# Kernel tuning notes

Hardware: AMD Instinct MI355X
Metric: run time of the kernel (lower is better)

Reference implementation:

```python
import jax, jax.numpy as jnp
import numpy as np


def setup_inputs() -> dict:
    key = jax.random.key(0)
    k1, k2 = jax.random.split(key)
    B, N, D = 16, 2048, 256
    candidate_vector = jax.random.normal(k1, (B, N, D), dtype=jnp.float32)
    # lengths in [1, N] so every softmax row has at least one valid column
    length = jax.random.randint(k2, (B,), 1, N + 1, dtype=jnp.int64)
    return {"candidate_vector": candidate_vector, "length": length}


def reference(candidate_vector, length):
    # scores[b,i,j] = <x_bi, x_bj>   (B, N, N)
    scores = jnp.einsum('bid,bjd->bij', candidate_vector, candidate_vector)
    # torch mask: mask[b,i,j] = (j < length[b]) -> columns past length masked
    N = candidate_vector.shape[1]
    col_valid = jnp.arange(N)[None, None, :] < length[:, None, None]  # (B,1,N)->(B,N,N) broadcast
    scores = jnp.where(col_valid, scores, -jnp.inf)
    weights = jax.nn.softmax(scores, axis=2)
    return jnp.einsum('bij,bjd->bid', weights, candidate_vector)
```

## Files before the change

### kernel.cpp

```cpp
#include <hip/hip_runtime.h>
#include <hip/hip_fp16.h>
#include <math.h>

typedef _Float16 f16;
typedef __attribute__((ext_vector_type(8))) _Float16 f16x8;
typedef __attribute__((ext_vector_type(4))) _Float16 f16x4;
typedef __attribute__((ext_vector_type(4))) float f32x4;
typedef unsigned int u32;
typedef unsigned long long u64;

#define NB 16
#define NN 2048
#define ND 256
#define KVB 32
#define QB 64
#define XSZ ((size_t)NB * NN * ND)

__device__ __forceinline__ void gll16(const void* g, void* l) {
    __builtin_amdgcn_global_load_lds(
        (const __attribute__((address_space(1))) unsigned int*)g,
        (__attribute__((address_space(3))) unsigned int*)l, 16, 0, 0);
}

__device__ __forceinline__ long long len_at(const int* lenp, int b, bool is64) {
    return is64 ? ((const long long*)lenp)[b] : (long long)lenp[b];
}

__device__ __forceinline__ float bperm_f(int src_lane, float v) {
    return __int_as_float(__builtin_amdgcn_ds_bpermute(src_lane * 4, __float_as_int(v)));
}

__global__ __launch_bounds__(256)
void prep(const float* __restrict__ X, f16* __restrict__ Xh, f16* __restrict__ Xt)
{
    const int b  = blockIdx.z;
    const int n0 = blockIdx.x * 64;
    const int d0 = blockIdx.y * 64;
    const int t  = threadIdx.x;
    __shared__ f16 T[64][72];

    const float* Xb  = X  + ((size_t)b*NN + n0)*ND + d0;
    f16*         Xhb = Xh + ((size_t)b*NN + n0)*ND + d0;
    #pragma unroll
    for (int it = 0; it < 4; ++it) {
        int r  = it*16 + (t >> 4);
        int c4 = t & 15;
        float4 v = *(const float4*)(Xb + (size_t)r*ND + c4*4);
        f16x4 h; h[0]=(f16)v.x; h[1]=(f16)v.y; h[2]=(f16)v.z; h[3]=(f16)v.w;
        *(f16x4*)&Xhb[(size_t)r*ND + c4*4] = h;
        *(f16x4*)&T[r][c4*4] = h;
    }
    __syncthreads();
    f16* Xtb = Xt + ((size_t)b*ND + d0)*NN + n0;
    #pragma unroll
    for (int it = 0; it < 2; ++it) {
        int id = it*256 + t;
        int dr = id >> 3;
        int ch = id & 7;
        f16x8 v;
        #pragma unroll
        for (int u = 0; u < 8; ++u) v[u] = T[ch*8+u][dr];
        *(f16x8*)&Xtb[(size_t)dr*NN + ch*8] = v;
    }
}

__global__ __launch_bounds__(256, 2)
void attn12(const f16* __restrict__ Xh, const f16* __restrict__ Xt,
            const int* __restrict__ lenp,
            f16* __restrict__ Op, float* __restrict__ Sl)
{
    const int tid  = threadIdx.x;
    const int lane = tid & 63;
    const int w = tid >> 6;
    const int g = lane >> 4;
    const int c = lane & 15;

    const bool is64 = (lenp[1] == 0);
    long long Lv[NB];
    #pragma unroll
    for (int i = 0; i < NB; ++i) Lv[i] = len_at(lenp, i, is64);
    const int x   = blockIdx.x & 7;
    const int kk2 = blockIdx.x >> 3;
    const int h   = kk2 & 1;
    const int k2  = kk2 >> 1;
    const int wanted = (k2 < 32) ? x : (15 - x);
    const int qt  = k2 & 31;
    int bsel = 0; long long Lb = 1;
    #pragma unroll
    for (int bb = 0; bb < NB; ++bb) {
        int rk = 0;
        #pragma unroll
        for (int b2 = 0; b2 < NB; ++b2)
            rk += (Lv[b2] > Lv[bb]) || (Lv[b2] == Lv[bb] && b2 < bb);
        if (rk == wanted) { bsel = bb; Lb = Lv[bb]; }
    }
    const int nt  = (int)((Lb + KVB - 1) / KVB);
    const int nth = (h == 0) ? ((nt + 1) >> 1) : (nt >> 1);
    if (nth == 0) return;

    __shared__ f16 Kl[8192];
    __shared__ f16 Vl[8192];
    __shared__ f16 Pl[4][16*40];

    const char* xhb = (const char*)(Xh + (size_t)bsel*NN*ND);
    const char* xtb = (const char*)(Xt + (size_t)bsel*ND*NN);

    f16x8 qf[8];
    {
        const char* qp = xhb + (size_t)(qt*QB + w*16 + c)*512 + g*16;
        const f16 LOG2E = (f16)1.44269504f;
        #pragma unroll
        for (int kk = 0; kk < 8; ++kk) {
            f16x8 v = *(const f16x8*)(qp + kk*64);
            qf[kk] = v * LOG2E;
        }
    }

    u64   ksrc[4], vsrc[4];
    char* kdst[4];
    char* vdst[4];
    {
        #pragma unroll
        for (int it = 0; it < 4; ++it) {
            int S  = it*256 + tid;
            int kk = S >> 7, j = (S >> 2) & 31, gg = S & 3;
            ksrc[it] = (u64)(xhb + (size_t)(h*KVB + j)*512 + kk*64 + gg*16);
            kdst[it] = (char*)&Kl[0] + S*16;
            int dt = S >> 6, cc = (S >> 2) & 15, g2 = S & 3;
            vsrc[it] = (u64)(xtb + (size_t)(dt*16 + cc)*4096 + (size_t)(h*KVB + g2*8)*2);
            vdst[it] = (char*)&Vl[0] + S*16;
        }
    }
    auto stage_k = [&]() {
        #pragma unroll
        for (int it = 0; it < 4; ++it) {
            gll16((const void*)ksrc[it], kdst[it]);
            ksrc[it] += (u64)(2*KVB*512);
        }
    };
    auto stage_v = [&]() {
        #pragma unroll
        for (int it = 0; it < 4; ++it) {
            gll16((const void*)vsrc[it], vdst[it]);
            vsrc[it] += (u64)(2*KVB*2);
        }
    };

    f32x4 o[16];
    #pragma unroll
    for (int dt = 0; dt < 16; ++dt) o[dt] = (f32x4){0.f,0.f,0.f,0.f};
    float m = -INFINITY;
    float l = 0.f;

    f16* pw = &Pl[w][0];

    stage_k();
    stage_v();

    for (int ti = 0; ti < nth; ++ti) {
        const int kv0 = (2*ti + h) * KVB;
        const bool more = (ti + 1 < nth);

        asm volatile("s_waitcnt vmcnt(4)" ::: "memory");
        __builtin_amdgcn_s_barrier();

        const char* kb = (const char*)&Kl[0];
        const char* vb = (const char*)&Vl[0];

        f32x4 s0 = (f32x4){0.f,0.f,0.f,0.f};
        f32x4 s1 = (f32x4){0.f,0.f,0.f,0.f};
        __builtin_amdgcn_s_setprio(1);
        #pragma unroll
        for (int kk = 0; kk < 8; ++kk) {
            f16x8 b0 = *(const f16x8*)(kb + kk*2048        + c*64 + g*16);
            f16x8 b1 = *(const f16x8*)(kb + kk*2048 + 1024 + c*64 + g*16);
            s0 = __builtin_amdgcn_mfma_f32_16x16x32_f16(b0, qf[kk], s0, 0, 0, 0);
            s1 = __builtin_amdgcn_mfma_f32_16x16x32_f16(b1, qf[kk], s1, 0, 0, 0);
        }
        __builtin_amdgcn_s_setprio(0);

        asm volatile("s_waitcnt vmcnt(0)" ::: "memory");
        __builtin_amdgcn_s_barrier();
        if (more) stage_k();

        const float NEG = -1e30f;
        if (kv0 + KVB > (int)Lb) {
            const int jb = kv0 + g*4;
            #pragma unroll
            for (int r = 0; r < 4; ++r) {
                if (jb + r >= Lb)      s0[r] = NEG;
                if (jb + 16 + r >= Lb) s1[r] = NEG;
            }
        }

        float tm = fmaxf(fmaxf(fmaxf(s0[0],s0[1]), fmaxf(s0[2],s0[3])),
                         fmaxf(fmaxf(s1[0],s1[1]), fmaxf(s1[2],s1[3])));
        tm = fmaxf(tm, __shfl_xor(tm, 16, 64));
        tm = fmaxf(tm, __shfl_xor(tm, 32, 64));
        if (__any(tm > m + 11.54f)) {
            float mn = fmaxf(m, tm);
            float sc = exp2f(m - mn);
            m = mn; l *= sc;
            float scr[4];
            #pragma unroll
            for (int r = 0; r < 4; ++r) scr[r] = bperm_f(g*4 + r, sc);
            #pragma unroll
            for (int dt = 0; dt < 16; ++dt) {
                o[dt][0]*=scr[0]; o[dt][1]*=scr[1]; o[dt][2]*=scr[2]; o[dt][3]*=scr[3];
            }
        }
        float p0[4], p1[4];
        #pragma unroll
        for (int r = 0; r < 4; ++r) {
            p0[r] = exp2f(s0[r] - m);
            p1[r] = exp2f(s1[r] - m);
        }
        float rs = ((p0[0]+p0[1]) + (p0[2]+p0[3])) + ((p1[0]+p1[1]) + (p1[2]+p1[3]));
        rs += __shfl_xor(rs, 16, 64);
        rs += __shfl_xor(rs, 32, 64);
        l += rs;

        f16x4 pa, pb;
        pa[0]=(f16)p0[0]; pa[1]=(f16)p0[1]; pa[2]=(f16)p0[2]; pa[3]=(f16)p0[3];
        pb[0]=(f16)p1[0]; pb[1]=(f16)p1[1]; pb[2]=(f16)p1[2]; pb[3]=(f16)p1[3];
        *(f16x4*)&pw[c*40 + 4*g]      = pa;
        *(f16x4*)&pw[c*40 + 16 + 4*g] = pb;
        f16x8 pf = *(const f16x8*)&pw[c*40 + 8*g];

        __builtin_amdgcn_s_setprio(1);
        #pragma unroll
        for (int dt = 0; dt < 16; ++dt) {
            f16x8 vf = *(const f16x8*)(vb + dt*1024 + c*64 + g*16);
            o[dt] = __builtin_amdgcn_mfma_f32_16x16x32_f16(pf, vf, o[dt], 0, 0, 0);
        }
        __builtin_amdgcn_s_setprio(0);

        asm volatile("" ::: "memory");
        __builtin_amdgcn_s_barrier();
        if (more) stage_v();
    }

    float linv = 1.f / l;
    float inv[4];
    #pragma unroll
    for (int r = 0; r < 4; ++r) inv[r] = bperm_f(g*4 + r, linv);
    f16* op = Op + (size_t)h*XSZ + ((size_t)bsel*NN + (size_t)(qt*QB + w*16 + g*4))*ND + c;
    #pragma unroll
    for (int r = 0; r < 4; ++r) {
        #pragma unroll
        for (int dt = 0; dt < 16; ++dt)
            op[(size_t)r*ND + dt*16] = (f16)(o[dt][r] * inv[r]);
    }
    if (g == 0) {
        Sl[((size_t)(h*NB + bsel))*NN + (size_t)(qt*QB + w*16 + c)] = m + log2f(l);
    }
}

__global__ __launch_bounds__(256)
void merge(const f16* __restrict__ Op, const float* __restrict__ Sl,
           const int* __restrict__ lenp, float* __restrict__ out)
{
    const int tid = threadIdx.x;
    const int rg  = blockIdx.x * 8 + (tid >> 5);
    const int b   = rg >> 11;
    const int q   = rg & 2047;
    const int d0  = (tid & 31) * 8;

    const bool is64 = (lenp[1] == 0);
    const long long Lb = len_at(lenp, b, is64);

    const f16* p1 = Op + ((size_t)b*NN + q)*ND + d0;
    f16x8 a1 = *(const f16x8*)p1;
    float r[8];
    if (Lb <= KVB) {
        #pragma unroll
        for (int i = 0; i < 8; ++i) r[i] = (float)a1[i];
    } else {
        f16x8 a2 = *(const f16x8*)(p1 + XSZ);
        float s1 = Sl[(size_t)b*NN + q];
        float s2 = Sl[(size_t)(NB + b)*NN + q];
        float sm = fmaxf(s1, s2);
        float w1 = exp2f(s1 - sm), w2 = exp2f(s2 - sm);
        float dn = 1.f / (w1 + w2);
        w1 *= dn; w2 *= dn;
        #pragma unroll
        for (int i = 0; i < 8; ++i) r[i] = (float)a1[i]*w1 + (float)a2[i]*w2;
    }
    float* ob = out + ((size_t)b*NN + q)*ND + d0;
    *(float4*)ob       = (float4){r[0], r[1], r[2], r[3]};
    *(float4*)(ob + 4) = (float4){r[4], r[5], r[6], r[7]};
}

__global__ __launch_bounds__(256, 2)
void attn4(const f16* __restrict__ Xh, const f16* __restrict__ Xt,
           const int* __restrict__ lenp, float* __restrict__ out)
{
    const int tid  = threadIdx.x;
    const int lane = tid & 63;
    const int w = tid >> 6;
    const int g = lane >> 4;
    const int c = lane & 15;

    const bool is64 = (lenp[1] == 0);
    long long Lv[NB];
    #pragma unroll
    for (int i = 0; i < NB; ++i) Lv[i] = len_at(lenp, i, is64);
    const int x = blockIdx.x & 7;
    const int k = blockIdx.x >> 3;
    const int wanted = (k < 32) ? x : (15 - x);
    const int qt = k & 31;
    int bsel = 0; long long Lb = 1;
    #pragma unroll
    for (int bb = 0; bb < NB; ++bb) {
        int rk = 0;
        #pragma unroll
        for (int b2 = 0; b2 < NB; ++b2)
            rk += (Lv[b2] > Lv[bb]) || (Lv[b2] == Lv[bb] && b2 < bb);
        if (rk == wanted) { bsel = bb; Lb = Lv[bb]; }
    }
    const int nt = (int)((Lb + KVB - 1) / KVB);

    __shared__ f16 Kl[2][8192];
    __shared__ f16 Vl[2][8192];
    __shared__ f16 Pl[4][16*36];

    const char* xhb = (const char*)(Xh + (size_t)bsel*NN*ND);
    const char* xtb = (const char*)(Xt + (size_t)bsel*ND*NN);

    f16x8 qf[8];
    {
        const char* qp = xhb + (size_t)(qt*QB + w*16 + c)*512 + g*16;
        #pragma unroll
        for (int kk = 0; kk < 8; ++kk) qf[kk] = *(const f16x8*)(qp + kk*64);
    }

    auto stage = [&](int buf, int kv0) {
        char* kb = (char*)&Kl[buf][0];
        char* vb = (char*)&Vl[buf][0];
        #pragma unroll
        for (int it = 0; it < 4; ++it) {
            int S  = it*256 + tid;
            int kk = S >> 7, j = (S >> 2) & 31, gg = S & 3;
            gll16(xhb + (size_t)(kv0 + j)*512 + kk*64 + gg*16, kb + S*16);
        }
        #pragma unroll
        for (int it = 0; it < 4; ++it) {
            int T  = it*256 + tid;
            int dt = T >> 6, cc = (T >> 2) & 15, gg = T & 3;
            gll16(xtb + (size_t)(dt*16 + cc)*4096 + (size_t)(kv0 + gg*8)*2, vb + T*16);
        }
    };

    f32x4 o[16];
    #pragma unroll
    for (int dt = 0; dt < 16; ++dt) o[dt] = (f32x4){0.f,0.f,0.f,0.f};
    float m[4] = {-INFINITY,-INFINITY,-INFINITY,-INFINITY};
    float l[4] = {0.f,0.f,0.f,0.f};

    f16* pw = &Pl[w][0];

    stage(0, 0);
    if (nt > 1) stage(1, KVB);

    for (int t = 0; t < nt; ++t) {
        const int kv0 = t * KVB;
        const int buf = t & 1;

        if (t + 1 < nt) { asm volatile("s_waitcnt vmcnt(8)" ::: "memory"); }
        else            { asm volatile("s_waitcnt vmcnt(0)" ::: "memory"); }
        __builtin_amdgcn_s_barrier();

        const char* kb = (const char*)&Kl[buf][0];
        const char* vb = (const char*)&Vl[buf][0];

        f32x4 s0 = (f32x4){0.f,0.f,0.f,0.f};
        f32x4 s1 = (f32x4){0.f,0.f,0.f,0.f};
        #pragma unroll
        for (int kk = 0; kk < 8; ++kk) {
            f16x8 b0 = *(const f16x8*)(kb + kk*2048        + c*64 + g*16);
            f16x8 b1 = *(const f16x8*)(kb + kk*2048 + 1024 + c*64 + g*16);
            s0 = __builtin_amdgcn_mfma_f32_16x16x32_f16(qf[kk], b0, s0, 0, 0, 0);
            s1 = __builtin_amdgcn_mfma_f32_16x16x32_f16(qf[kk], b1, s1, 0, 0, 0);
        }

        const float NEG = -1e30f;
        if (kv0 + c >= Lb)      { s0[0]=NEG; s0[1]=NEG; s0[2]=NEG; s0[3]=NEG; }
        if (kv0 + 16 + c >= Lb) { s1[0]=NEG; s1[1]=NEG; s1[2]=NEG; s1[3]=NEG; }

        float mx[4], mn[4], sc[4], p0[4], p1[4], rs[4];
        #pragma unroll
        for (int r = 0; r < 4; ++r) mx[r] = fmaxf(s0[r], s1[r]);
        #pragma unroll
        for (int off = 8; off >= 1; off >>= 1) {
            #pragma unroll
            for (int r = 0; r < 4; ++r)
                mx[r] = fmaxf(mx[r], __shfl_xor(mx[r], off, 64));
        }
        #pragma unroll
        for (int r = 0; r < 4; ++r) {
            mn[r] = fmaxf(m[r], mx[r]);
            sc[r] = __expf(m[r] - mn[r]);
            p0[r] = __expf(s0[r] - mn[r]);
            p1[r] = __expf(s1[r] - mn[r]);
            rs[r] = p0[r] + p1[r];
        }
        #pragma unroll
        for (int off = 8; off >= 1; off >>= 1) {
            #pragma unroll
            for (int r = 0; r < 4; ++r)
                rs[r] += __shfl_xor(rs[r], off, 64);
        }
        bool chg = (sc[0]!=1.f) | (sc[1]!=1.f) | (sc[2]!=1.f) | (sc[3]!=1.f);
        if (__any(chg)) {
            #pragma unroll
            for (int dt = 0; dt < 16; ++dt) {
                o[dt][0]*=sc[0]; o[dt][1]*=sc[1]; o[dt][2]*=sc[2]; o[dt][3]*=sc[3];
            }
        }
        #pragma unroll
        for (int r = 0; r < 4; ++r) { l[r] = l[r]*sc[r] + rs[r]; m[r] = mn[r]; }

        #pragma unroll
        for (int r = 0; r < 4; ++r) {
            pw[(g*4+r)*36 + c]      = (f16)p0[r];
            pw[(g*4+r)*36 + 16 + c] = (f16)p1[r];
        }
        union { f16x4 hh[2]; f16x8 v; } pu;
        pu.hh[0] = *(const f16x4*)(pw + c*36 + g*8);
        pu.hh[1] = *(const f16x4*)(pw + c*36 + g*8 + 4);
        f16x8 pf = pu.v;

        #pragma unroll
        for (int dt = 0; dt < 16; ++dt) {
            f16x8 vf = *(const f16x8*)(vb + dt*1024 + c*64 + g*16);
            o[dt] = __builtin_amdgcn_mfma_f32_16x16x32_f16(pf, vf, o[dt], 0, 0, 0);
        }

        __builtin_amdgcn_s_barrier();
        if (t + 2 < nt) stage(buf, kv0 + 2*KVB);
    }

    float inv[4];
    #pragma unroll
    for (int r = 0; r < 4; ++r) inv[r] = 1.0f / l[r];
    float* ob = out + ((size_t)bsel*NN + (size_t)(qt*QB + w*16 + g*4))*ND + c;
    #pragma unroll
    for (int r = 0; r < 4; ++r) {
        #pragma unroll
        for (int dt = 0; dt < 16; ++dt)
            ob[(size_t)r*ND + dt*16] = o[dt][r] * inv[r];
    }
}

__global__ __launch_bounds__(256, 2)
void attn_fb(const float* __restrict__ X,
             const int* __restrict__ lenp,
             float* __restrict__ out)
{
    const int b   = blockIdx.y;
    const int qt  = blockIdx.x;
    const int tid = threadIdx.x;
    const int lane = tid & 63;
    const int w = tid >> 6;
    const int g = lane >> 4;
    const int c = lane & 15;

    const bool is64 = (lenp[1] == 0);
    const long long Lb = len_at(lenp, b, is64);

    __shared__ f16 Kl[KVB][264];
    __shared__ f16 Vt2[ND][40];
    __shared__ f16 Pl[4][16][40];

    const float* Xb = X + (size_t)b * NN * ND;

    f16x8 qf[8];
    {
        const float* qp = Xb + (size_t)(qt*64 + w*16 + c) * ND + g*8;
        #pragma unroll
        for (int kk = 0; kk < 8; ++kk) {
            float4 a = *(const float4*)(qp + kk*32);
            float4 d = *(const float4*)(qp + kk*32 + 4);
            f16x8 v;
            v[0]=(f16)a.x; v[1]=(f16)a.y; v[2]=(f16)a.z; v[3]=(f16)a.w;
            v[4]=(f16)d.x; v[5]=(f16)d.y; v[6]=(f16)d.z; v[7]=(f16)d.w;
            qf[kk] = v;
        }
    }

    f32x4 o[16];
    #pragma unroll
    for (int dt = 0; dt < 16; ++dt) o[dt] = (f32x4){0.f,0.f,0.f,0.f};
    float m[4] = {-INFINITY,-INFINITY,-INFINITY,-INFINITY};
    float lr[4] = {0.f,0.f,0.f,0.f};

    const int ntiles = (int)((Lb + KVB - 1) / KVB);
    for (int t = 0; t < ntiles; ++t) {
        const int kv0 = t * KVB;
        __syncthreads();
        #pragma unroll
        for (int it = 0; it < 8; ++it) {
            int idx4 = it*256 + tid;
            int row  = idx4 >> 6;
            int c4   = idx4 & 63;
            float4 v = *(const float4*)(Xb + (size_t)(kv0 + row)*ND + c4*4);
            f16x4 hh; hh[0]=(f16)v.x; hh[1]=(f16)v.y; hh[2]=(f16)v.z; hh[3]=(f16)v.w;
            *(f16x4*)&Kl[row][c4*4] = hh;
        }
        {
            const float* cp = Xb + (size_t)kv0*ND + tid;
            #pragma unroll
            for (int kq = 0; kq < 8; ++kq) {
                f16x4 hh;
                #pragma unroll
                for (int u = 0; u < 4; ++u) hh[u] = (f16)cp[(size_t)(kq*4+u)*ND];
                *(f16x4*)&Vt2[tid][kq*4] = hh;
            }
        }
        __syncthreads();

        f32x4 s0 = (f32x4){0.f,0.f,0.f,0.f};
        f32x4 s1 = (f32x4){0.f,0.f,0.f,0.f};
        #pragma unroll
        for (int kk = 0; kk < 8; ++kk) {
            f16x8 b0 = *(const f16x8*)&Kl[c     ][kk*32 + g*8];
            f16x8 b1 = *(const f16x8*)&Kl[16 + c][kk*32 + g*8];
            s0 = __builtin_amdgcn_mfma_f32_16x16x32_f16(qf[kk], b0, s0, 0, 0, 0);
            s1 = __builtin_amdgcn_mfma_f32_16x16x32_f16(qf[kk], b1, s1, 0, 0, 0);
        }

        const float NEG = -1e30f;
        if (kv0 + c >= Lb)      { s0[0]=NEG; s0[1]=NEG; s0[2]=NEG; s0[3]=NEG; }
        if (kv0 + 16 + c >= Lb) { s1[0]=NEG; s1[1]=NEG; s1[2]=NEG; s1[3]=NEG; }

        float mx[4], mn[4], sc[4], p0[4], p1[4], rs[4];
        #pragma unroll
        for (int r = 0; r < 4; ++r) mx[r] = fmaxf(s0[r], s1[r]);
        #pragma unroll
        for (int off = 8; off >= 1; off >>= 1) {
            #pragma unroll
            for (int r = 0; r < 4; ++r)
                mx[r] = fmaxf(mx[r], __shfl_xor(mx[r], off, 64));
        }
        #pragma unroll
        for (int r = 0; r < 4; ++r) {
            mn[r] = fmaxf(m[r], mx[r]);
            sc[r] = __expf(m[r] - mn[r]);
            p0[r] = __expf(s0[r] - mn[r]);
            p1[r] = __expf(s1[r] - mn[r]);
            rs[r] = p0[r] + p1[r];
        }
        #pragma unroll
        for (int off = 8; off >= 1; off >>= 1) {
            #pragma unroll
            for (int r = 0; r < 4; ++r)
                rs[r] += __shfl_xor(rs[r], off, 64);
        }
        bool chg = (sc[0]!=1.f) | (sc[1]!=1.f) | (sc[2]!=1.f) | (sc[3]!=1.f);
        if (__any(chg)) {
            #pragma unroll
            for (int dt = 0; dt < 16; ++dt) {
                o[dt][0]*=sc[0]; o[dt][1]*=sc[1]; o[dt][2]*=sc[2]; o[dt][3]*=sc[3];
            }
        }
        #pragma unroll
        for (int r = 0; r < 4; ++r) { lr[r] = lr[r]*sc[r] + rs[r]; m[r] = mn[r]; }

        #pragma unroll
        for (int r = 0; r < 4; ++r) {
            Pl[w][g*4+r][c]      = (f16)p0[r];
            Pl[w][g*4+r][16 + c] = (f16)p1[r];
        }
        f16x8 pf = *(const f16x8*)&Pl[w][c][g*8];

        #pragma unroll
        for (int dt = 0; dt < 16; ++dt) {
            f16x8 vf = *(const f16x8*)&Vt2[dt*16 + c][g*8];
            o[dt] = __builtin_amdgcn_mfma_f32_16x16x32_f16(pf, vf, o[dt], 0, 0, 0);
        }
    }

    float inv[4];
    #pragma unroll
    for (int r = 0; r < 4; ++r) inv[r] = 1.0f / lr[r];
    float* ob = out + ((size_t)b*NN + (size_t)(qt*64 + w*16 + g*4))*ND + c;
    #pragma unroll
    for (int r = 0; r < 4; ++r) {
        #pragma unroll
        for (int dt = 0; dt < 16; ++dt)
            ob[(size_t)r*ND + dt*16] = o[dt][r] * inv[r];
    }
}

extern "C" void kernel_launch(void* const* d_in, const int* in_sizes, int n_in,
                              void* d_out, int out_size, void* d_ws, size_t ws_size,
                              hipStream_t stream) {
    const float* X    = (const float*)d_in[0];
    const int*   lenp = (const int*)d_in[1];
    float*       out  = (float*)d_out;

    const size_t need_base  = XSZ * 2 * 2;
    const size_t need_split = need_base + XSZ * 2 * 2
                              + (size_t)2 * NB * NN * 4;
    if (ws_size >= need_split) {
        f16* Xh = (f16*)d_ws;
        f16* Xt = Xh + XSZ;
        f16* Op = Xt + XSZ;
        float* Sl = (float*)(Op + 2*XSZ);
        hipLaunchKernelGGL(prep, dim3(NN/64, ND/64, NB), dim3(256), 0, stream, X, Xh, Xt);
        hipLaunchKernelGGL(attn12, dim3(1024), dim3(256), 0, stream, Xh, Xt, lenp, Op, Sl);
        hipLaunchKernelGGL(merge, dim3(NB*NN/8), dim3(256), 0, stream, Op, Sl, lenp, out);
    } else if (ws_size >= need_base) {
        f16* Xh = (f16*)d_ws;
        f16* Xt = Xh + XSZ;
        hipLaunchKernelGGL(prep, dim3(NN/64, ND/64, NB), dim3(256), 0, stream, X, Xh, Xt);
        hipLaunchKernelGGL(attn4, dim3(512), dim3(256), 0, stream, Xh, Xt, lenp, out);
    } else {
        hipLaunchKernelGGL(attn_fb, dim3(NN/64, NB), dim3(256), 0, stream, X, lenp, out);
    }
}
```

Baseline: 97.57 us.

## Split KV range three ways with single-buffered attention and three-way merge

Adds attn13, which splits each query tile's KV sequence across three interleaved workgroups (1536 blocks), with a merge3 kernel that combines the partial outputs using their log-sum-exp values. Inside the kernel it computes the transposed S tile so each lane owns one query row, folds log2e into Q, and skips the rescale unless the max grows past a threshold (lazy rescale). P is moved between lanes with ds_bpermute instead of going through LDS, K and V are single-buffered with split waits, and MFMA sections get raised priority. It aims for better occupancy and load balance but needs more workspace, writes more partial outputs, and the old attn4 path is removed.

Measured after the change: 101.0 us. 1.04x slower.

```diff
diff --git a/kernel.cpp b/kernel.cpp
--- a/kernel.cpp
+++ b/kernel.cpp
@@ -62,6 +62,255 @@
         for (int u = 0; u < 8; ++u) v[u] = T[ch*8+u][dr];
         *(f16x8*)&Xtb[(size_t)dr*NN + ch*8] = v;
     }
+}
+
+__global__ __launch_bounds__(256, 2)
+void attn13(const f16* __restrict__ Xh, const f16* __restrict__ Xt,
+            const int* __restrict__ lenp,
+            f16* __restrict__ Op, float* __restrict__ Sl)
+{
+    const int tid  = threadIdx.x;
+    const int lane = tid & 63;
+    const int w = tid >> 6;
+    const int g = lane >> 4;
+    const int c = lane & 15;
+
+    const bool is64 = (lenp[1] == 0);
+    long long Lv[NB];
+    #pragma unroll
+    for (int i = 0; i < NB; ++i) Lv[i] = len_at(lenp, i, is64);
+    const int x   = blockIdx.x & 7;
+    const int k   = blockIdx.x >> 3;
+    const int wanted = (k < 96) ? x : (15 - x);
+    const int rem = (k < 96) ? k : (k - 96);
+    const int qt  = rem & 31;
+    const int h   = rem >> 5;
+    int bsel = 0; long long Lb = 1;
+    #pragma unroll
+    for (int bb = 0; bb < NB; ++bb) {
+        int rk = 0;
+        #pragma unroll
+        for (int b2 = 0; b2 < NB; ++b2)
+            rk += (Lv[b2] > Lv[bb]) || (Lv[b2] == Lv[bb] && b2 < bb);
+        if (rk == wanted) { bsel = bb; Lb = Lv[bb]; }
+    }
+    const int nt  = (int)((Lb + KVB - 1) / KVB);
+    const int nth = (nt - h + 2) / 3;
+    if (nth <= 0) return;
+
+    __shared__ f16 Kl[8192];
+    __shared__ f16 Vl[8192];
+
+    const char* xhb = (const char*)(Xh + (size_t)bsel*NN*ND);
+    const char* xtb = (const char*)(Xt + (size_t)bsel*ND*NN);
+
+    f16x8 qf[8];
+    {
+        const char* qp = xhb + (size_t)(qt*QB + w*16 + c)*512 + g*16;
+        const f16 LOG2E = (f16)1.44269504f;
+        #pragma unroll
+        for (int kk = 0; kk < 8; ++kk) {
+            f16x8 v = *(const f16x8*)(qp + kk*64);
+            qf[kk] = v * LOG2E;
+        }
+    }
+
+    u64   ksrc[4], vsrc[4];
+    char* kdst[4];
+    char* vdst[4];
+    {
+        #pragma unroll
+        for (int it = 0; it < 4; ++it) {
+            int S  = it*256 + tid;
+            int kk = S >> 7, j = (S >> 2) & 31, gg = S & 3;
+            ksrc[it] = (u64)(xhb + (size_t)(h*KVB + j)*512 + kk*64 + gg*16);
+            kdst[it] = (char*)&Kl[0] + S*16;
+            int dt = S >> 6, cc = (S >> 2) & 15, g2 = S & 3;
+            vsrc[it] = (u64)(xtb + (size_t)(dt*16 + cc)*4096 + (size_t)(h*KVB + g2*8)*2);
+            vdst[it] = (char*)&Vl[0] + S*16;
+        }
+    }
+    auto stage_k = [&]() {
+        #pragma unroll
+        for (int it = 0; it < 4; ++it) {
+            gll16((const void*)ksrc[it], kdst[it]);
+            ksrc[it] += (u64)(3*KVB*512);
+        }
+    };
+    auto stage_v = [&]() {
+        #pragma unroll
+        for (int it = 0; it < 4; ++it) {
+            gll16((const void*)vsrc[it], vdst[it]);
+            vsrc[it] += (u64)(3*KVB*2);
+        }
+    };
+
+    f32x4 o[16];
+    #pragma unroll
+    for (int dt = 0; dt < 16; ++dt) o[dt] = (f32x4){0.f,0.f,0.f,0.f};
+    float m = -INFINITY;
+    float l = 0.f;
+
+    stage_k();
+    stage_v();
+
+    for (int ti = 0; ti < nth; ++ti) {
+        const int kv0 = (3*ti + h) * KVB;
+        const bool more = (ti + 1 < nth);
+
+        asm volatile("s_waitcnt vmcnt(4)" ::: "memory");
+        __builtin_amdgcn_s_barrier();
+
+        const char* kb = (const char*)&Kl[0];
+        const char* vb = (const char*)&Vl[0];
+
+        f32x4 s0 = (f32x4){0.f,0.f,0.f,0.f};
+        f32x4 s1 = (f32x4){0.f,0.f,0.f,0.f};
+        __builtin_amdgcn_s_setprio(1);
+        #pragma unroll
+        for (int kk = 0; kk < 8; ++kk) {
+            f16x8 b0 = *(const f16x8*)(kb + kk*2048        + c*64 + g*16);
+            f16x8 b1 = *(const f16x8*)(kb + kk*2048 + 1024 + c*64 + g*16);
+            s0 = __builtin_amdgcn_mfma_f32_16x16x32_f16(b0, qf[kk], s0, 0, 0, 0);
+            s1 = __builtin_amdgcn_mfma_f32_16x16x32_f16(b1, qf[kk], s1, 0, 0, 0);
+        }
+        __builtin_amdgcn_s_setprio(0);
+
+        asm volatile("s_waitcnt vmcnt(0)" ::: "memory");
+        __builtin_amdgcn_s_barrier();
+        if (more) stage_k();
+
+        const float NEG = -1e30f;
+        if (kv0 + KVB > (int)Lb) {
+            const int jb = kv0 + g*4;
+            #pragma unroll
+            for (int r = 0; r < 4; ++r) {
+                if (jb + r >= Lb)      s0[r] = NEG;
+                if (jb + 16 + r >= Lb) s1[r] = NEG;
+            }
+        }
+
+        float tm = fmaxf(fmaxf(fmaxf(s0[0],s0[1]), fmaxf(s0[2],s0[3])),
+                         fmaxf(fmaxf(s1[0],s1[1]), fmaxf(s1[2],s1[3])));
+        tm = fmaxf(tm, __shfl_xor(tm, 16, 64));
+        tm = fmaxf(tm, __shfl_xor(tm, 32, 64));
+        if (__any(tm > m + 11.54f)) {
+            float mn = fmaxf(m, tm);
+            float sc = exp2f(m - mn);
+            m = mn; l *= sc;
+            float scr[4];
+            #pragma unroll
+            for (int r = 0; r < 4; ++r) scr[r] = bperm_f(g*4 + r, sc);
+            #pragma unroll
+            for (int dt = 0; dt < 16; ++dt) {
+                o[dt][0]*=scr[0]; o[dt][1]*=scr[1]; o[dt][2]*=scr[2]; o[dt][3]*=scr[3];
+            }
+        }
+        float p0[4], p1[4];
+        #pragma unroll
+        for (int r = 0; r < 4; ++r) {
+            p0[r] = exp2f(s0[r] - m);
+            p1[r] = exp2f(s1[r] - m);
+        }
+        float rs = ((p0[0]+p0[1]) + (p0[2]+p0[3])) + ((p1[0]+p1[1]) + (p1[2]+p1[3]));
+        rs += __shfl_xor(rs, 16, 64);
+        rs += __shfl_xor(rs, 32, 64);
+        l += rs;
+
+        f16x4 pa, pb;
+        pa[0]=(f16)p0[0]; pa[1]=(f16)p0[1]; pa[2]=(f16)p0[2]; pa[3]=(f16)p0[3];
+        pb[0]=(f16)p1[0]; pb[1]=(f16)p1[1]; pb[2]=(f16)p1[2]; pb[3]=(f16)p1[3];
+        u32 a0 = ((u32*)&pa)[0], a1 = ((u32*)&pa)[1];
+        u32 b0_ = ((u32*)&pb)[0], b1_ = ((u32*)&pb)[1];
+        const bool lo = (g < 2);
+        const int gA   = lo ? (2*g) : (2*g - 4);
+        const int adrA = (gA*16 + c) * 4;
+        const int adrB = adrA + 64;
+        u32 xA0 = __builtin_amdgcn_ds_bpermute(adrA, a0);
+        u32 xA1 = __builtin_amdgcn_ds_bpermute(adrA, a1);
+        u32 yA0 = __builtin_amdgcn_ds_bpermute(adrA, b0_);
+        u32 yA1 = __builtin_amdgcn_ds_bpermute(adrA, b1_);
+        u32 xB0 = __builtin_amdgcn_ds_bpermute(adrB, a0);
+        u32 xB1 = __builtin_amdgcn_ds_bpermute(adrB, a1);
+        u32 yB0 = __builtin_amdgcn_ds_bpermute(adrB, b0_);
+        u32 yB1 = __builtin_amdgcn_ds_bpermute(adrB, b1_);
+        union { u32 u[4]; f16x8 v; } pf;
+        pf.u[0] = lo ? xA0 : yA0;
+        pf.u[1] = lo ? xA1 : yA1;
+        pf.u[2] = lo ? xB0 : yB0;
+        pf.u[3] = lo ? xB1 : yB1;
+
+        __builtin_amdgcn_s_setprio(1);
+        #pragma unroll
+        for (int dt = 0; dt < 16; ++dt) {
+            f16x8 vf = *(const f16x8*)(vb + dt*1024 + c*64 + g*16);
+            o[dt] = __builtin_amdgcn_mfma_f32_16x16x32_f16(pf.v, vf, o[dt], 0, 0, 0);
+        }
+        __builtin_amdgcn_s_setprio(0);
+
+        asm volatile("" ::: "memory");
+        __builtin_amdgcn_s_barrier();
+        if (more) stage_v();
+    }
+
+    float linv = 1.f / l;
+    float inv[4];
+    #pragma unroll
+    for (int r = 0; r < 4; ++r) inv[r] = bperm_f(g*4 + r, linv);
+    f16* op = Op + (size_t)h*XSZ + ((size_t)bsel*NN + (size_t)(qt*QB + w*16 + g*4))*ND + c;
+    #pragma unroll
+    for (int r = 0; r < 4; ++r) {
+        #pragma unroll
+        for (int dt = 0; dt < 16; ++dt)
+            op[(size_t)r*ND + dt*16] = (f16)(o[dt][r] * inv[r]);
+    }
+    if (g == 0) {
+        Sl[((size_t)(h*NB + bsel))*NN + (size_t)(qt*QB + w*16 + c)] = m + log2f(l);
+    }
+}
+
+__global__ __launch_bounds__(256)
+void merge3(const f16* __restrict__ Op, const float* __restrict__ Sl,
+            const int* __restrict__ lenp, float* __restrict__ out)
+{
+    const int tid = threadIdx.x;
+    const int rg  = blockIdx.x * 8 + (tid >> 5);
+    const int b   = rg >> 11;
+    const int q   = rg & 2047;
+    const int d0  = (tid & 31) * 8;
+
+    const bool is64 = (lenp[1] == 0);
+    const long long Lb = len_at(lenp, b, is64);
+    const bool v1 = (Lb > KVB);
+    const bool v2 = (Lb > 2*KVB);
+
+    const f16* p0 = Op + ((size_t)b*NN + q)*ND + d0;
+    f16x8 a0 = *(const f16x8*)p0;
+    float r[8];
+    if (!v1) {
+        #pragma unroll
+        for (int i = 0; i < 8; ++i) r[i] = (float)a0[i];
+    } else {
+        float s0 = Sl[(size_t)b*NN + q];
+        float s1 = Sl[(size_t)(NB + b)*NN + q];
+        float s2 = v2 ? Sl[(size_t)(2*NB + b)*NN + q] : -INFINITY;
+        float sm = fmaxf(fmaxf(s0, s1), s2);
+        float w0 = exp2f(s0 - sm), w1 = exp2f(s1 - sm);
+        float w2 = v2 ? exp2f(s2 - sm) : 0.f;
+        float dn = 1.f / (w0 + w1 + w2);
+        w0 *= dn; w1 *= dn; w2 *= dn;
+        f16x8 a1 = *(const f16x8*)(p0 + XSZ);
+        #pragma unroll
+        for (int i = 0; i < 8; ++i) r[i] = (float)a0[i]*w0 + (float)a1[i]*w1;
+        if (v2) {
+            f16x8 a2 = *(const f16x8*)(p0 + 2*XSZ);
+            #pragma unroll
+            for (int i = 0; i < 8; ++i) r[i] += (float)a2[i]*w2;
+        }
+    }
+    float* ob = out + ((size_t)b*NN + q)*ND + d0;
+    *(float4*)ob       = (float4){r[0], r[1], r[2], r[3]};
+    *(float4*)(ob + 4) = (float4){r[4], r[5], r[6], r[7]};
 }
 
 __global__ __launch_bounds__(256, 2)
@@ -289,167 +538,6 @@
     float* ob = out + ((size_t)b*NN + q)*ND + d0;
     *(float4*)ob       = (float4){r[0], r[1], r[2], r[3]};
     *(float4*)(ob + 4) = (float4){r[4], r[5], r[6], r[7]};
-}
-
-__global__ __launch_bounds__(256, 2)
-void attn4(const f16* __restrict__ Xh, const f16* __restrict__ Xt,
-           const int* __restrict__ lenp, float* __restrict__ out)
-{
-    const int tid  = threadIdx.x;
-    const int lane = tid & 63;
-    const int w = tid >> 6;
-    const int g = lane >> 4;
-    const int c = lane & 15;
-
-    const bool is64 = (lenp[1] == 0);
-    long long Lv[NB];
-    #pragma unroll
-    for (int i = 0; i < NB; ++i) Lv[i] = len_at(lenp, i, is64);
-    const int x = blockIdx.x & 7;
-    const int k = blockIdx.x >> 3;
-    const int wanted = (k < 32) ? x : (15 - x);
-    const int qt = k & 31;
-    int bsel = 0; long long Lb = 1;
-    #pragma unroll
-    for (int bb = 0; bb < NB; ++bb) {
-        int rk = 0;
-        #pragma unroll
-        for (int b2 = 0; b2 < NB; ++b2)
-            rk += (Lv[b2] > Lv[bb]) || (Lv[b2] == Lv[bb] && b2 < bb);
-        if (rk == wanted) { bsel = bb; Lb = Lv[bb]; }
-    }
-    const int nt = (int)((Lb + KVB - 1) / KVB);
-
-    __shared__ f16 Kl[2][8192];
-    __shared__ f16 Vl[2][8192];
-    __shared__ f16 Pl[4][16*36];
-
-    const char* xhb = (const char*)(Xh + (size_t)bsel*NN*ND);
-    const char* xtb = (const char*)(Xt + (size_t)bsel*ND*NN);
-
-    f16x8 qf[8];
-    {
-        const char* qp = xhb + (size_t)(qt*QB + w*16 + c)*512 + g*16;
-        #pragma unroll
-        for (int kk = 0; kk < 8; ++kk) qf[kk] = *(const f16x8*)(qp + kk*64);
-    }
-
-    auto stage = [&](int buf, int kv0) {
-        char* kb = (char*)&Kl[buf][0];
-        char* vb = (char*)&Vl[buf][0];
-        #pragma unroll
-        for (int it = 0; it < 4; ++it) {
-            int S  = it*256 + tid;
-            int kk = S >> 7, j = (S >> 2) & 31, gg = S & 3;
-            gll16(xhb + (size_t)(kv0 + j)*512 + kk*64 + gg*16, kb + S*16);
-        }
-        #pragma unroll
-        for (int it = 0; it < 4; ++it) {
-            int T  = it*256 + tid;
-            int dt = T >> 6, cc = (T >> 2) & 15, gg = T & 3;
-            gll16(xtb + (size_t)(dt*16 + cc)*4096 + (size_t)(kv0 + gg*8)*2, vb + T*16);
-        }
-    };
-
-    f32x4 o[16];
-    #pragma unroll
-    for (int dt = 0; dt < 16; ++dt) o[dt] = (f32x4){0.f,0.f,0.f,0.f};
-    float m[4] = {-INFINITY,-INFINITY,-INFINITY,-INFINITY};
-    float l[4] = {0.f,0.f,0.f,0.f};
-
-    f16* pw = &Pl[w][0];
-
-    stage(0, 0);
-    if (nt > 1) stage(1, KVB);
-
-    for (int t = 0; t < nt; ++t) {
-        const int kv0 = t * KVB;
-        const int buf = t & 1;
-
-        if (t + 1 < nt) { asm volatile("s_waitcnt vmcnt(8)" ::: "memory"); }
-        else            { asm volatile("s_waitcnt vmcnt(0)" ::: "memory"); }
-        __builtin_amdgcn_s_barrier();
-
-        const char* kb = (const char*)&Kl[buf][0];
-        const char* vb = (const char*)&Vl[buf][0];
-
-        f32x4 s0 = (f32x4){0.f,0.f,0.f,0.f};
-        f32x4 s1 = (f32x4){0.f,0.f,0.f,0.f};
-        #pragma unroll
-        for (int kk = 0; kk < 8; ++kk) {
-            f16x8 b0 = *(const f16x8*)(kb + kk*2048        + c*64 + g*16);
-            f16x8 b1 = *(const f16x8*)(kb + kk*2048 + 1024 + c*64 + g*16);
-            s0 = __builtin_amdgcn_mfma_f32_16x16x32_f16(qf[kk], b0, s0, 0, 0, 0);
-            s1 = __builtin_amdgcn_mfma_f32_16x16x32_f16(qf[kk], b1, s1, 0, 0, 0);
-        }
-
-        const float NEG = -1e30f;
-        if (kv0 + c >= Lb)      { s0[0]=NEG; s0[1]=NEG; s0[2]=NEG; s0[3]=NEG; }
-        if (kv0 + 16 + c >= Lb) { s1[0]=NEG; s1[1]=NEG; s1[2]=NEG; s1[3]=NEG; }
-
-        float mx[4], mn[4], sc[4], p0[4], p1[4], rs[4];
-        #pragma unroll
-        for (int r = 0; r < 4; ++r) mx[r] = fmaxf(s0[r], s1[r]);
-        #pragma unroll
-        for (int off = 8; off >= 1; off >>= 1) {
-            #pragma unroll
-            for (int r = 0; r < 4; ++r)
-                mx[r] = fmaxf(mx[r], __shfl_xor(mx[r], off, 64));
-        }
-        #pragma unroll
-        for (int r = 0; r < 4; ++r) {
-            mn[r] = fmaxf(m[r], mx[r]);
-            sc[r] = __expf(m[r] - mn[r]);
-            p0[r] = __expf(s0[r] - mn[r]);
-            p1[r] = __expf(s1[r] - mn[r]);
-            rs[r] = p0[r] + p1[r];
-        }
-        #pragma unroll
-        for (int off = 8; off >= 1; off >>= 1) {
-            #pragma unroll
-            for (int r = 0; r < 4; ++r)
-                rs[r] += __shfl_xor(rs[r], off, 64);
-        }
-        bool chg = (sc[0]!=1.f) | (sc[1]!=1.f) | (sc[2]!=1.f) | (sc[3]!=1.f);
-        if (__any(chg)) {
-            #pragma unroll
-            for (int dt = 0; dt < 16; ++dt) {
-                o[dt][0]*=sc[0]; o[dt][1]*=sc[1]; o[dt][2]*=sc[2]; o[dt][3]*=sc[3];
-            }
-        }
-        #pragma unroll
-        for (int r = 0; r < 4; ++r) { l[r] = l[r]*sc[r] + rs[r]; m[r] = mn[r]; }
-
-        #pragma unroll
-        for (int r = 0; r < 4; ++r) {
-            pw[(g*4+r)*36 + c]      = (f16)p0[r];
-            pw[(g*4+r)*36 + 16 + c] = (f16)p1[r];
-        }
-        union { f16x4 hh[2]; f16x8 v; } pu;
-        pu.hh[0] = *(const f16x4*)(pw + c*36 + g*8);
-        pu.hh[1] = *(const f16x4*)(pw + c*36 + g*8 + 4);
-        f16x8 pf = pu.v;
-
-        #pragma unroll
-        for (int dt = 0; dt < 16; ++dt) {
-            f16x8 vf = *(const f16x8*)(vb + dt*1024 + c*64 + g*16);
-            o[dt] = __builtin_amdgcn_mfma_f32_16x16x32_f16(pf, vf, o[dt], 0, 0, 0);
-        }
-
-        __builtin_amdgcn_s_barrier();
-        if (t + 2 < nt) stage(buf, kv0 + 2*KVB);
-    }
-
-    float inv[4];
-    #pragma unroll
-    for (int r = 0; r < 4; ++r) inv[r] = 1.0f / l[r];
-    float* ob = out + ((size_t)bsel*NN + (size_t)(qt*QB + w*16 + g*4))*ND + c;
-    #pragma unroll
-    for (int r = 0; r < 4; ++r) {
-        #pragma unroll
-        for (int dt = 0; dt < 16; ++dt)
-            ob[(size_t)r*ND + dt*16] = o[dt][r] * inv[r];
-    }
 }
 
 __global__ __launch_bounds__(256, 2)
@@ -599,10 +687,20 @@
     const int*   lenp = (const int*)d_in[1];
     float*       out  = (float*)d_out;
 
-    const size_t need_base  = XSZ * 2 * 2;
-    const size_t need_split = need_base + XSZ * 2 * 2
-                              + (size_t)2 * NB * NN * 4;
-    if (ws_size >= need_split) {
+    const size_t need_base   = XSZ * 2 * 2;
+    const size_t need_split2 = need_base + XSZ * 2 * 2
+                               + (size_t)2 * NB * NN * 4;
+    const size_t need_split3 = need_base + XSZ * 3 * 2
+                               + (size_t)3 * NB * NN * 4;
+    if (ws_size >= need_split3) {
+        f16* Xh = (f16*)d_ws;
+        f16* Xt = Xh + XSZ;
+        f16* Op = Xt + XSZ;
+        float* Sl = (float*)(Op + 3*XSZ);
+        hipLaunchKernelGGL(prep, dim3(NN/64, ND/64, NB), dim3(256), 0, stream, X, Xh, Xt);
+        hipLaunchKernelGGL(attn13, dim3(1536), dim3(256), 0, stream, Xh, Xt, lenp, Op, Sl);
+        hipLaunchKernelGGL(merge3, dim3(NB*NN/8), dim3(256), 0, stream, Op, Sl, lenp, out);
+    } else if (ws_size >= need_split2) {
         f16* Xh = (f16*)d_ws;
         f16* Xt = Xh + XSZ;
         f16* Op = Xt + XSZ;
@@ -610,11 +708,6 @@
         hipLaunchKernelGGL(prep, dim3(NN/64, ND/64, NB), dim3(256), 0, stream, X, Xh, Xt);
         hipLaunchKernelGGL(attn12, dim3(1024), dim3(256), 0, stream, Xh, Xt, lenp, Op, Sl);
         hipLaunchKernelGGL(merge, dim3(NB*NN/8), dim3(256), 0, stream, Op, Sl, lenp, out);
-    } else if (ws_size >= need_base) {
-        f16* Xh = (f16*)d_ws;
-        f16* Xt = Xh + XSZ;
-        hipLaunchKernelGGL(prep, dim3(NN/64, ND/64, NB), dim3(256), 0, stream, X, Xh, Xt);
-        hipLaunchKernelGGL(attn4, dim3(512), dim3(256), 0, stream, Xh, Xt, lenp, out);
     } else {
         hipLaunchKernelGGL(attn_fb, dim3(NN/64, NB), dim3(256), 0, stream, X, lenp, out);
     }
```
